# Kernel tuning notes

Measured on AMD Instinct MI355X. Metric: run time of the kernel, lower is better.

The kernel has to match this reference:

```python
import jax, jax.numpy as jnp
import numpy as np

N_ELEC = 64
IN_C = 64
HID = [64, 128]
OUT_C = 128
BATCH = 2048
BN_EPS = 1e-5


def build_graph():
    """Replicates EEGGraphNet._build_graph_structure with random 3D electrode positions."""
    rng = np.random.RandomState(0)
    pos = rng.rand(N_ELEC, 3).astype(np.float64)
    d = np.sqrt(((pos[:, None, :] - pos[None, :, :]) ** 2).sum(-1))
    thr = np.percentile(d[d > 0], 30)
    src, dst = [], []
    for i in range(N_ELEC):
        for j in range(i + 1, N_ELEC):
            if d[i, j] < thr:
                src += [i, j]
                dst += [j, i]
    return np.asarray(src, np.int32), np.asarray(dst, np.int32)


def setup_inputs() -> dict:
    key = jax.random.key(0)
    ks = jax.random.split(key, 8)
    src, dst = build_graph()
    dims = [IN_C] + HID + [OUT_C]  # [64, 64, 128, 128]
    inp = {"x": jax.random.normal(ks[0], (BATCH, N_ELEC, IN_C), jnp.float32)}
    for li in range(3):
        fi, fo = dims[li], dims[li + 1]
        inp[f"W{li+1}"] = jax.random.normal(ks[li + 1], (fi, fo), jnp.float32) * (1.0 / np.sqrt(fi))
        inp[f"b{li+1}"] = jnp.zeros((fo,), jnp.float32)
    for li in range(2):  # BN after first two convs
        inp[f"g{li+1}"] = jnp.ones((dims[li + 1],), jnp.float32)
        inp[f"be{li+1}"] = jnp.zeros((dims[li + 1],), jnp.float32)
    inp["src"] = jnp.asarray(src)
    inp["dst"] = jnp.asarray(dst)
    return inp


def gcn_conv(x, W, b, src, dst, edge_norm, self_norm):
    # x: (B, N, Fin) -> (B, N, Fout). GCN with self-loops, symmetric norm.
    h = jnp.einsum("bnf,fo->bno", x, W)
    msg = h[:, src, :] * edge_norm[None, :, None]          # (B, E, Fout) gather
    agg = jnp.zeros_like(h).at[:, dst, :].add(msg)         # scatter-add over dst
    return agg + h * self_norm[None, :, None] + b


def batchnorm(x, g, be):
    # torch BatchNorm1d over flattened (B*N, C) nodes, training-mode batch stats
    m = jnp.mean(x, axis=(0, 1))
    v = jnp.mean((x - m) ** 2, axis=(0, 1))
    return g * (x - m) * jax.lax.rsqrt(v + BN_EPS) + be


def reference(x, W1, b1, W2, b2, W3, b3, g1, be1, g2, be2, src, dst):
    # degree (with self-loop) is identical across graphs in the batch
    deg = jnp.zeros((N_ELEC,), x.dtype).at[dst].add(1.0) + 1.0
    inv_sqrt = jax.lax.rsqrt(deg)
    edge_norm = inv_sqrt[src] * inv_sqrt[dst]
    self_norm = 1.0 / deg

    h = gcn_conv(x, W1, b1, src, dst, edge_norm, self_norm)
    h = jax.nn.relu(batchnorm(h, g1, be1))
    h = gcn_conv(h, W2, b2, src, dst, edge_norm, self_norm)
    h = jax.nn.relu(batchnorm(h, g2, be2))
    h = gcn_conv(h, W3, b3, src, dst, edge_norm, self_norm)
    return jnp.mean(h, axis=1)  # global mean pool over electrodes -> (B, OUT_C)
```

## Files before the change

kernel.cpp:

```cpp
#include <hip/hip_runtime.h>
#include <hip/hip_bf16.h>

typedef unsigned short ushortT;
typedef unsigned int uintT;
typedef __attribute__((ext_vector_type(8))) short short8;
typedef __attribute__((ext_vector_type(4))) float f32x4;

#define BATCH   2048
#define NELEC   64
#define BN_EPS  1e-5f

#define OFF_AMEAN  4096
#define OFF_SS1    4160
#define OFF_SS2    4288
#define OFF_PS1    4544
#define OFF_PQ1    8640
#define OFF_PS2    12736
#define OFF_PQ2    20928
#define UOFF_A     0
#define UOFF_W1T   9216
#define UOFF_W2T   18432
#define UOFF_H1    36864
#define UOFF_H2    (36864 + 8388608)

#define MFMA(a, b, c) __builtin_amdgcn_mfma_f32_16x16x32_bf16(a, b, c, 0, 0, 0)

__device__ inline float bf2f(ushortT u) { return __uint_as_float(((uintT)u) << 16); }
__device__ inline ushortT f2bf(float f) {
  uintT u = __float_as_uint(f);
  u = (u + 0x7FFFu + ((u >> 16) & 1u)) >> 16;
  return (ushortT)u;
}
__device__ inline void split2(float f, ushortT& hi, ushortT& lo) {
  hi = f2bf(f);
  lo = f2bf(f - bf2f(hi));
}
__device__ inline void splitT8(const float* f, short8& hi, short8& lo) {
  #pragma unroll
  for (int e = 0; e < 8; ++e) {
    uintT u = __float_as_uint(f[e]);
    float fh = __uint_as_float(u & 0xFFFF0000u);
    hi[e] = (short)(u >> 16);
    lo[e] = (short)f2bf(f[e] - fh);
  }
}
__device__ inline uint2 pack4(f32x4 v) {
  uint2 pk;
  pk.x = (uintT)f2bf(v[0]) | ((uintT)f2bf(v[1]) << 16);
  pk.y = (uintT)f2bf(v[2]) | ((uintT)f2bf(v[3]) << 16);
  return pk;
}

__global__ __launch_bounds__(256) void prep_kernel(const int* __restrict__ src,
    const int* __restrict__ dst, int E,
    const float* __restrict__ W1, const float* __restrict__ W2,
    float* __restrict__ ws) {
  __shared__ float degS[NELEC];
  __shared__ float As[NELEC * NELEC];
  int t = threadIdx.x;
  if (t < NELEC) degS[t] = 1.0f;
  for (int i = t; i < NELEC * NELEC; i += 256) As[i] = 0.0f;
  __syncthreads();
  for (int e = t; e < E; e += 256) atomicAdd(&degS[dst[e]], 1.0f);
  __syncthreads();
  for (int e = t; e < E; e += 256) {
    float en = rsqrtf(degS[src[e]]) * rsqrtf(degS[dst[e]]);
    atomicAdd(&As[dst[e] * NELEC + src[e]], en);
  }
  __syncthreads();
  if (t < NELEC) As[t * NELEC + t] += 1.0f / degS[t];
  __syncthreads();
  ushortT* U = (ushortT*)(ws + 29120);
  ushortT* a72 = U + UOFF_A;
  for (int i = t; i < 4096; i += 256) {
    int row = i >> 6, k = i & 63;
    ushortT hi, lo; split2(As[i], hi, lo);
    a72[row * 72 + k] = hi; a72[4608 + row * 72 + k] = lo;
  }
  if (t < NELEC) {
    float s = 0.0f;
    for (int n = 0; n < NELEC; ++n) s += As[n * NELEC + t];
    ws[OFF_AMEAN + t] = s * (1.0f / NELEC);
  }
  ushortT* w1t = U + UOFF_W1T;
  for (int i = t; i < 4096; i += 256) {
    int o = i >> 6, k = i & 63;
    ushortT hi, lo; split2(W1[k * 64 + o], hi, lo);
    w1t[o * 72 + k] = hi; w1t[4608 + o * 72 + k] = lo;
  }
  ushortT* w2t = U + UOFF_W2T;
  for (int i = t; i < 8192; i += 256) {
    int o = i >> 6, k = i & 63;
    ushortT hi, lo; split2(W2[k * 128 + o], hi, lo);
    w2t[o * 72 + k] = hi; w2t[9216 + o * 72 + k] = lo;
  }
}

__global__ __launch_bounds__(512, 2) void layer1_fused(const float* __restrict__ x,
    const float* __restrict__ b1, float* __restrict__ ws) {
  __shared__ ushortT Wl[9216];
  __shared__ ushortT Tt[36864];
  const int t = threadIdx.x;
  ushortT* U = (ushortT*)(ws + 29120);
  for (int i = t; i < 1152; i += 512)
    ((uint4*)Wl)[i] = ((const uint4*)(U + UOFF_W1T))[i];
  const int w = t >> 6, lane = t & 63, c = lane & 15, g = lane >> 4;
  const int b = blockIdx.x * 8 + w;
  short8 Xh[4][2], Xl[4][2];
  #pragma unroll
  for (int nq = 0; nq < 4; ++nq) {
    #pragma unroll
    for (int ks = 0; ks < 2; ++ks) {
      const float* p = x + (size_t)b * 4096 + (nq * 16 + c) * 64 + ks * 32 + g * 8;
      float4 fa = *(const float4*)p, fb = *(const float4*)(p + 4);
      float f[8] = {fa.x, fa.y, fa.z, fa.w, fb.x, fb.y, fb.z, fb.w};
      splitT8(f, Xh[nq][ks], Xl[nq][ks]);
    }
  }
  __syncthreads();
  f32x4 acc[4][4];
  #pragma unroll
  for (int i = 0; i < 4; ++i)
    #pragma unroll
    for (int j = 0; j < 4; ++j) acc[i][j] = (f32x4){0.f, 0.f, 0.f, 0.f};
  #pragma unroll
  for (int ot = 0; ot < 4; ++ot) {
    #pragma unroll
    for (int ks = 0; ks < 2; ++ks) {
      short8 bh = *(const short8*)&Wl[(ot * 16 + c) * 72 + ks * 32 + g * 8];
      short8 bl = *(const short8*)&Wl[4608 + (ot * 16 + c) * 72 + ks * 32 + g * 8];
      #pragma unroll
      for (int nq = 0; nq < 4; ++nq) {
        acc[nq][ot] = MFMA(Xh[nq][ks], bh, acc[nq][ot]);
        acc[nq][ot] = MFMA(Xh[nq][ks], bl, acc[nq][ot]);
        acc[nq][ot] = MFMA(Xl[nq][ks], bh, acc[nq][ot]);
      }
    }
  }
  ushortT* tt = &Tt[w * 4608];
  #pragma unroll
  for (int ot = 0; ot < 4; ++ot)
    #pragma unroll
    for (int nq = 0; nq < 4; ++nq)
      *(uint2*)&tt[(ot * 16 + c) * 72 + nq * 16 + 4 * g] = pack4(acc[nq][ot]);
  short8 ABh[4][2], ABl[4][2];
  #pragma unroll
  for (int sp = 0; sp < 4; ++sp)
    #pragma unroll
    for (int ks = 0; ks < 2; ++ks) {
      ABh[sp][ks] = *(const short8*)(U + (sp * 16 + c) * 72 + ks * 32 + g * 8);
      ABl[sp][ks] = *(const short8*)(U + 4608 + (sp * 16 + c) * 72 + ks * 32 + g * 8);
    }
  f32x4 h[4][4];
  #pragma unroll
  for (int i = 0; i < 4; ++i)
    #pragma unroll
    for (int j = 0; j < 4; ++j) h[i][j] = (f32x4){0.f, 0.f, 0.f, 0.f};
  #pragma unroll
  for (int ks = 0; ks < 2; ++ks) {
    short8 af[4];
    #pragma unroll
    for (int rt = 0; rt < 4; ++rt)
      af[rt] = *(const short8*)&tt[(rt * 16 + c) * 72 + ks * 32 + g * 8];
    #pragma unroll
    for (int sp = 0; sp < 4; ++sp)
      #pragma unroll
      for (int rt = 0; rt < 4; ++rt) {
        h[rt][sp] = MFMA(af[rt], ABh[sp][ks], h[rt][sp]);
        h[rt][sp] = MFMA(af[rt], ABl[sp][ks], h[rt][sp]);
      }
  }
  float Sa[4][4], Qa[4][4];
  #pragma unroll
  for (int i = 0; i < 4; ++i)
    #pragma unroll
    for (int j = 0; j < 4; ++j) { Sa[i][j] = 0.f; Qa[i][j] = 0.f; }
  #pragma unroll
  for (int rt = 0; rt < 4; ++rt) {
    float4 bv = *(const float4*)(b1 + rt * 16 + 4 * g);
    #pragma unroll
    for (int sp = 0; sp < 4; ++sp) {
      f32x4 v;
      v[0] = h[rt][sp][0] + bv.x; v[1] = h[rt][sp][1] + bv.y;
      v[2] = h[rt][sp][2] + bv.z; v[3] = h[rt][sp][3] + bv.w;
      Sa[rt][0] += v[0]; Qa[rt][0] += v[0] * v[0];
      Sa[rt][1] += v[1]; Qa[rt][1] += v[1] * v[1];
      Sa[rt][2] += v[2]; Qa[rt][2] += v[2] * v[2];
      Sa[rt][3] += v[3]; Qa[rt][3] += v[3] * v[3];
      *(uint2*)&tt[(sp * 16 + c) * 72 + rt * 16 + 4 * g] = pack4(v);
    }
  }
  const int slot = blockIdx.x & 63;
  #pragma unroll
  for (int rt = 0; rt < 4; ++rt)
    #pragma unroll
    for (int r = 0; r < 4; ++r) {
      float S = Sa[rt][r], Q = Qa[rt][r];
      S += __shfl_xor(S, 1); S += __shfl_xor(S, 2); S += __shfl_xor(S, 4); S += __shfl_xor(S, 8);
      Q += __shfl_xor(Q, 1); Q += __shfl_xor(Q, 2); Q += __shfl_xor(Q, 4); Q += __shfl_xor(Q, 8);
      if (c == 0) {
        atomicAdd(&ws[OFF_PS1 + slot * 64 + rt * 16 + 4 * g + r], S);
        atomicAdd(&ws[OFF_PQ1 + slot * 64 + rt * 16 + 4 * g + r], Q);
      }
    }
  __syncthreads();
  {
    const int ib = t >> 6, n2 = t & 63;
    const uint4* srcp = (const uint4*)&Tt[ib * 4608 + n2 * 72];
    uint4* dstp = (uint4*)(U + UOFF_H1 + (size_t)(blockIdx.x * 8 + ib) * 4096 + n2 * 64);
    #pragma unroll
    for (int j = 0; j < 8; ++j) dstp[j] = srcp[j];
  }
}

__global__ void reduce1_kernel(const float* __restrict__ g1, const float* __restrict__ be1,
                               float* __restrict__ ws) {
  int t = threadIdx.x;
  if (t < 64) {
    float S = 0.0f, Q = 0.0f;
    for (int s = 0; s < 64; ++s) { S += ws[OFF_PS1 + s * 64 + t]; Q += ws[OFF_PQ1 + s * 64 + t]; }
    const float inv = 1.0f / (float)(BATCH * NELEC);
    float m = S * inv;
    float v = fmaxf(Q * inv - m * m, 0.0f);
    float sc = g1[t] * rsqrtf(v + BN_EPS);
    ws[OFF_SS1 + t] = sc;
    ws[OFF_SS1 + 64 + t] = fmaf(-m, sc, be1[t]);
  }
}

__global__ void reduce2_kernel(const float* __restrict__ g2, const float* __restrict__ be2,
                               float* __restrict__ ws) {
  int t = threadIdx.x;
  if (t < 128) {
    float S = 0.0f, Q = 0.0f;
    for (int s = 0; s < 64; ++s) { S += ws[OFF_PS2 + s * 128 + t]; Q += ws[OFF_PQ2 + s * 128 + t]; }
    const float inv = 1.0f / (float)(BATCH * NELEC);
    float m = S * inv;
    float v = fmaxf(Q * inv - m * m, 0.0f);
    float sc = g2[t] * rsqrtf(v + BN_EPS);
    ws[OFF_SS2 + t] = sc;
    ws[OFF_SS2 + 128 + t] = fmaf(-m, sc, be2[t]);
  }
}

__global__ __launch_bounds__(512, 2) void layer2_fused(const float* __restrict__ b2,
    float* __restrict__ ws) {
  __shared__ ushortT Wl[18432];
  __shared__ ushortT Tt[36864];
  const int t = threadIdx.x;
  ushortT* U = (ushortT*)(ws + 29120);
  for (int i = t; i < 2304; i += 512)
    ((uint4*)Wl)[i] = ((const uint4*)(U + UOFF_W2T))[i];
  const int w = t >> 6, lane = t & 63, c = lane & 15, g = lane >> 4;
  const int b0 = blockIdx.x * 4;
  const ushortT* h1g = U + UOFF_H1;
  float s8[2][8], t8[2][8];
  #pragma unroll
  for (int ks = 0; ks < 2; ++ks) {
    const float* sp_ = ws + OFF_SS1 + ks * 32 + g * 8;
    const float* tp_ = ws + OFF_SS1 + 64 + ks * 32 + g * 8;
    float4 sa = *(const float4*)sp_, sb = *(const float4*)(sp_ + 4);
    float4 ta = *(const float4*)tp_, tb = *(const float4*)(tp_ + 4);
    s8[ks][0]=sa.x; s8[ks][1]=sa.y; s8[ks][2]=sa.z; s8[ks][3]=sa.w;
    s8[ks][4]=sb.x; s8[ks][5]=sb.y; s8[ks][6]=sb.z; s8[ks][7]=sb.w;
    t8[ks][0]=ta.x; t8[ks][1]=ta.y; t8[ks][2]=ta.z; t8[ks][3]=ta.w;
    t8[ks][4]=tb.x; t8[ks][5]=tb.y; t8[ks][6]=tb.z; t8[ks][7]=tb.w;
  }
  short8 Yh[2][2], Yl[2][2];
  #pragma unroll
  for (int si = 0; si < 2; ++si) {
    const int sub = w * 2 + si, ib = sub >> 2, nq = sub & 3;
    #pragma unroll
    for (int ks = 0; ks < 2; ++ks) {
      short8 hv = *(const short8*)(h1g + (size_t)(b0 + ib) * 4096 + (nq * 16 + c) * 64 + ks * 32 + g * 8);
      float f[8];
      #pragma unroll
      for (int e = 0; e < 8; ++e)
        f[e] = fmaxf(fmaf(bf2f((ushortT)hv[e]), s8[ks][e], t8[ks][e]), 0.0f);
      splitT8(f, Yh[si][ks], Yl[si][ks]);
    }
  }
  __syncthreads();
  f32x4 acc[2][8];
  #pragma unroll
  for (int i = 0; i < 2; ++i)
    #pragma unroll
    for (int j = 0; j < 8; ++j) acc[i][j] = (f32x4){0.f, 0.f, 0.f, 0.f};
  #pragma unroll
  for (int ot = 0; ot < 8; ++ot) {
    #pragma unroll
    for (int ks = 0; ks < 2; ++ks) {
      short8 bh = *(const short8*)&Wl[(ot * 16 + c) * 72 + ks * 32 + g * 8];
      short8 bl = *(const short8*)&Wl[9216 + (ot * 16 + c) * 72 + ks * 32 + g * 8];
      #pragma unroll
      for (int si = 0; si < 2; ++si) {
        acc[si][ot] = MFMA(Yh[si][ks], bh, acc[si][ot]);
        acc[si][ot] = MFMA(Yh[si][ks], bl, acc[si][ot]);
        acc[si][ot] = MFMA(Yl[si][ks], bh, acc[si][ot]);
      }
    }
  }
  #pragma unroll
  for (int si = 0; si < 2; ++si) {
    const int sub = w * 2 + si, ib = sub >> 2, nq = sub & 3;
    #pragma unroll
    for (int ot = 0; ot < 8; ++ot)
      *(uint2*)&Tt[ib * 9216 + (ot * 16 + c) * 72 + nq * 16 + 4 * g] = pack4(acc[si][ot]);
  }
  short8 ABh[4][2], ABl[4][2];
  #pragma unroll
  for (int sp = 0; sp < 4; ++sp)
    #pragma unroll
    for (int ks = 0; ks < 2; ++ks) {
      ABh[sp][ks] = *(const short8*)(U + (sp * 16 + c) * 72 + ks * 32 + g * 8);
      ABl[sp][ks] = *(const short8*)(U + 4608 + (sp * 16 + c) * 72 + ks * 32 + g * 8);
    }
  __syncthreads();
  const int ib = w >> 1, oh = w & 1;
  const ushortT* tt = &Tt[ib * 9216];
  f32x4 h[4][4];
  #pragma unroll
  for (int i = 0; i < 4; ++i)
    #pragma unroll
    for (int j = 0; j < 4; ++j) h[i][j] = (f32x4){0.f, 0.f, 0.f, 0.f};
  #pragma unroll
  for (int ks = 0; ks < 2; ++ks) {
    short8 af[4];
    #pragma unroll
    for (int rt = 0; rt < 4; ++rt)
      af[rt] = *(const short8*)&tt[(oh * 64 + rt * 16 + c) * 72 + ks * 32 + g * 8];
    #pragma unroll
    for (int sp = 0; sp < 4; ++sp)
      #pragma unroll
      for (int rt = 0; rt < 4; ++rt) {
        h[rt][sp] = MFMA(af[rt], ABh[sp][ks], h[rt][sp]);
        h[rt][sp] = MFMA(af[rt], ABl[sp][ks], h[rt][sp]);
      }
  }
  float Sa[4][4], Qa[4][4];
  #pragma unroll
  for (int i = 0; i < 4; ++i)
    #pragma unroll
    for (int j = 0; j < 4; ++j) { Sa[i][j] = 0.f; Qa[i][j] = 0.f; }
  #pragma unroll
  for (int rt = 0; rt < 4; ++rt) {
    float4 bv = *(const float4*)(b2 + oh * 64 + rt * 16 + 4 * g);
    #pragma unroll
    for (int sp = 0; sp < 4; ++sp) {
      h[rt][sp][0] += bv.x; h[rt][sp][1] += bv.y;
      h[rt][sp][2] += bv.z; h[rt][sp][3] += bv.w;
      Sa[rt][0] += h[rt][sp][0]; Qa[rt][0] += h[rt][sp][0] * h[rt][sp][0];
      Sa[rt][1] += h[rt][sp][1]; Qa[rt][1] += h[rt][sp][1] * h[rt][sp][1];
      Sa[rt][2] += h[rt][sp][2]; Qa[rt][2] += h[rt][sp][2] * h[rt][sp][2];
      Sa[rt][3] += h[rt][sp][3]; Qa[rt][3] += h[rt][sp][3] * h[rt][sp][3];
    }
  }
  const int slot = blockIdx.x & 63;
  #pragma unroll
  for (int rt = 0; rt < 4; ++rt)
    #pragma unroll
    for (int r = 0; r < 4; ++r) {
      float S = Sa[rt][r], Q = Qa[rt][r];
      S += __shfl_xor(S, 1); S += __shfl_xor(S, 2); S += __shfl_xor(S, 4); S += __shfl_xor(S, 8);
      Q += __shfl_xor(Q, 1); Q += __shfl_xor(Q, 2); Q += __shfl_xor(Q, 4); Q += __shfl_xor(Q, 8);
      if (c == 0) {
        const int ch = oh * 64 + rt * 16 + 4 * g + r;
        atomicAdd(&ws[OFF_PS2 + slot * 128 + ch], S);
        atomicAdd(&ws[OFF_PQ2 + slot * 128 + ch], Q);
      }
    }
  __syncthreads();
  {
    ushortT* hb = &Tt[ib * 9216];
    #pragma unroll
    for (int rt = 0; rt < 4; ++rt)
      #pragma unroll
      for (int sp = 0; sp < 4; ++sp)
        *(uint2*)&hb[(sp * 16 + c) * 136 + oh * 64 + rt * 16 + 4 * g] = pack4(h[rt][sp]);
  }
  __syncthreads();
  {
    const int ib2 = t >> 7, n2 = (t >> 1) & 63, half = t & 1;
    const uint4* srcp = (const uint4*)&Tt[ib2 * 9216 + n2 * 136 + half * 64];
    uint4* dstp = (uint4*)(U + UOFF_H2 + (size_t)(b0 + ib2) * 8192 + n2 * 128 + half * 64);
    #pragma unroll
    for (int j = 0; j < 8; ++j) dstp[j] = srcp[j];
  }
}

__global__ __launch_bounds__(256) void layer3_kernel(const float* __restrict__ W3,
    const float* __restrict__ b3, const float* __restrict__ ws,
    float* __restrict__ out) {
  const int w = threadIdx.x >> 6, lane = threadIdx.x & 63;
  const int item = blockIdx.x * 4 + w;
  const int f0 = lane * 2;
  const float s2a = ws[OFF_SS2 + f0],       s2b = ws[OFF_SS2 + f0 + 1];
  const float t2a = ws[OFF_SS2 + 128 + f0], t2b = ws[OFF_SS2 + 128 + f0 + 1];
  const float* am = ws + OFF_AMEAN;
  const ushortT* h2 = (const ushortT*)(ws + 29120) + UOFF_H2 + (size_t)item * 8192;
  float v0 = 0.0f, v1 = 0.0f;
  #pragma unroll 8
  for (int m = 0; m < 64; ++m) {
    uintT pk = *(const uintT*)(h2 + m * 128 + f0);
    float y0 = fmaxf(fmaf(bf2f((ushortT)(pk & 0xffffu)), s2a, t2a), 0.0f);
    float y1 = fmaxf(fmaf(bf2f((ushortT)(pk >> 16)),     s2b, t2b), 0.0f);
    float a = am[m];
    v0 = fmaf(a, y0, v0);
    v1 = fmaf(a, y1, v1);
  }
  float o0 = b3[f0], o1 = b3[f0 + 1];
  #pragma unroll 8
  for (int k = 0; k < 128; ++k) {
    float vk = __shfl((k & 1) ? v1 : v0, k >> 1, 64);
    o0 = fmaf(vk, W3[k * 128 + f0],     o0);
    o1 = fmaf(vk, W3[k * 128 + f0 + 1], o1);
  }
  float2 ov; ov.x = o0; ov.y = o1;
  *(float2*)(out + (size_t)item * 128 + f0) = ov;
}

extern "C" void kernel_launch(void* const* d_in, const int* in_sizes, int n_in,
                              void* d_out, int out_size, void* d_ws, size_t ws_size,
                              hipStream_t stream) {
  const float* x   = (const float*)d_in[0];
  const float* W1  = (const float*)d_in[1];
  const float* b1  = (const float*)d_in[2];
  const float* W2  = (const float*)d_in[3];
  const float* b2  = (const float*)d_in[4];
  const float* W3  = (const float*)d_in[5];
  const float* b3  = (const float*)d_in[6];
  const float* g1  = (const float*)d_in[7];
  const float* be1 = (const float*)d_in[8];
  const float* g2  = (const float*)d_in[9];
  const float* be2 = (const float*)d_in[10];
  const int*   src = (const int*)d_in[11];
  const int*   dst = (const int*)d_in[12];
  const int E = in_sizes[11];
  float* ws  = (float*)d_ws;
  float* out = (float*)d_out;

  hipMemsetAsync((void*)(ws + OFF_PS1), 0, (size_t)(29120 - OFF_PS1) * 4, stream);
  hipLaunchKernelGGL(prep_kernel,    dim3(1),   dim3(256), 0, stream, src, dst, E, W1, W2, ws);
  hipLaunchKernelGGL(layer1_fused,   dim3(256), dim3(512), 0, stream, x, b1, ws);
  hipLaunchKernelGGL(reduce1_kernel, dim3(1),   dim3(64),  0, stream, g1, be1, ws);
  hipLaunchKernelGGL(layer2_fused,   dim3(512), dim3(512), 0, stream, b2, ws);
  hipLaunchKernelGGL(reduce2_kernel, dim3(1),   dim3(128), 0, stream, g2, be2, ws);
  hipLaunchKernelGGL(layer3_kernel,  dim3(512), dim3(256), 0, stream, W3, b3, ws, out);
}
```

Measured before the change: 186.2 us.

## Split fused GCN layers into separate weight-GEMM, adjacency-GEMM and stats kernels

Each fused layer kernel is split into three kernels. The first does the feature-weight GEMM and writes an intermediate bf16 tensor to global memory. The second does the adjacency GEMM plus bias. The third computes BatchNorm sums in a separate pass with a shared-memory reduction. The goal is smaller blocks with fewer registers and less LDS, giving higher occupancy and fewer atomics, at the cost of extra global round trips and more kernel launches. Layer 3 also stages its pooled vector through shared memory with vectorised W3 loads instead of using shuffles.

Result: slower. 195.6 us (+5.1%).

```diff
diff --git a/kernel.cpp b/kernel.cpp
--- a/kernel.cpp
+++ b/kernel.cpp
@@ -21,7 +21,9 @@
 #define UOFF_W1T   9216
 #define UOFF_W2T   18432
 #define UOFF_H1    36864
-#define UOFF_H2    (36864 + 8388608)
+#define UOFF_H2    8425472
+#define UOFF_T1    25202688
+#define UOFF_T2    25202688
 
 #define MFMA(a, b, c) __builtin_amdgcn_mfma_f32_16x16x32_bf16(a, b, c, 0, 0, 0)
 
@@ -96,31 +98,31 @@
   }
 }
 
-__global__ __launch_bounds__(512, 2) void layer1_fused(const float* __restrict__ x,
-    const float* __restrict__ b1, float* __restrict__ ws) {
+__global__ __launch_bounds__(256, 4) void wgemm1_kernel(const float* __restrict__ x,
+    float* __restrict__ ws) {
   __shared__ ushortT Wl[9216];
-  __shared__ ushortT Tt[36864];
   const int t = threadIdx.x;
   ushortT* U = (ushortT*)(ws + 29120);
-  for (int i = t; i < 1152; i += 512)
+  for (int i = t; i < 1152; i += 256)
     ((uint4*)Wl)[i] = ((const uint4*)(U + UOFF_W1T))[i];
   const int w = t >> 6, lane = t & 63, c = lane & 15, g = lane >> 4;
-  const int b = blockIdx.x * 8 + w;
-  short8 Xh[4][2], Xl[4][2];
-  #pragma unroll
-  for (int nq = 0; nq < 4; ++nq) {
-    #pragma unroll
-    for (int ks = 0; ks < 2; ++ks) {
-      const float* p = x + (size_t)b * 4096 + (nq * 16 + c) * 64 + ks * 32 + g * 8;
+  const int wv = blockIdx.x * 4 + w;
+  const int b = wv >> 1, nh = wv & 1;
+  short8 Xh[2][2], Xl[2][2];
+  #pragma unroll
+  for (int nq = 0; nq < 2; ++nq) {
+    #pragma unroll
+    for (int ks = 0; ks < 2; ++ks) {
+      const float* p = x + (size_t)b * 4096 + ((nh * 2 + nq) * 16 + c) * 64 + ks * 32 + g * 8;
       float4 fa = *(const float4*)p, fb = *(const float4*)(p + 4);
       float f[8] = {fa.x, fa.y, fa.z, fa.w, fb.x, fb.y, fb.z, fb.w};
       splitT8(f, Xh[nq][ks], Xl[nq][ks]);
     }
   }
   __syncthreads();
-  f32x4 acc[4][4];
-  #pragma unroll
-  for (int i = 0; i < 4; ++i)
+  f32x4 acc[2][4];
+  #pragma unroll
+  for (int i = 0; i < 2; ++i)
     #pragma unroll
     for (int j = 0; j < 4; ++j) acc[i][j] = (f32x4){0.f, 0.f, 0.f, 0.f};
   #pragma unroll
@@ -130,86 +132,92 @@
       short8 bh = *(const short8*)&Wl[(ot * 16 + c) * 72 + ks * 32 + g * 8];
       short8 bl = *(const short8*)&Wl[4608 + (ot * 16 + c) * 72 + ks * 32 + g * 8];
       #pragma unroll
-      for (int nq = 0; nq < 4; ++nq) {
+      for (int nq = 0; nq < 2; ++nq) {
         acc[nq][ot] = MFMA(Xh[nq][ks], bh, acc[nq][ot]);
         acc[nq][ot] = MFMA(Xh[nq][ks], bl, acc[nq][ot]);
         acc[nq][ot] = MFMA(Xl[nq][ks], bh, acc[nq][ot]);
       }
     }
   }
-  ushortT* tt = &Tt[w * 4608];
+  ushortT* t1 = U + UOFF_T1 + (size_t)b * 4096;
   #pragma unroll
   for (int ot = 0; ot < 4; ++ot)
     #pragma unroll
-    for (int nq = 0; nq < 4; ++nq)
-      *(uint2*)&tt[(ot * 16 + c) * 72 + nq * 16 + 4 * g] = pack4(acc[nq][ot]);
-  short8 ABh[4][2], ABl[4][2];
-  #pragma unroll
-  for (int sp = 0; sp < 4; ++sp)
-    #pragma unroll
-    for (int ks = 0; ks < 2; ++ks) {
-      ABh[sp][ks] = *(const short8*)(U + (sp * 16 + c) * 72 + ks * 32 + g * 8);
-      ABl[sp][ks] = *(const short8*)(U + 4608 + (sp * 16 + c) * 72 + ks * 32 + g * 8);
-    }
-  f32x4 h[4][4];
-  #pragma unroll
-  for (int i = 0; i < 4; ++i)
-    #pragma unroll
-    for (int j = 0; j < 4; ++j) h[i][j] = (f32x4){0.f, 0.f, 0.f, 0.f};
-  #pragma unroll
-  for (int ks = 0; ks < 2; ++ks) {
-    short8 af[4];
-    #pragma unroll
-    for (int rt = 0; rt < 4; ++rt)
-      af[rt] = *(const short8*)&tt[(rt * 16 + c) * 72 + ks * 32 + g * 8];
-    #pragma unroll
-    for (int sp = 0; sp < 4; ++sp)
+    for (int nq = 0; nq < 2; ++nq)
+      *(uint2*)&t1[(ot * 16 + c) * 64 + (nh * 2 + nq) * 16 + 4 * g] = pack4(acc[nq][ot]);
+}
+
+__global__ __launch_bounds__(256, 4) void agemm1_kernel(const float* __restrict__ b1,
+    float* __restrict__ ws) {
+  const int t = threadIdx.x, w = t >> 6, lane = t & 63, c = lane & 15, g = lane >> 4;
+  const int wv = blockIdx.x * 4 + w;
+  const int b = wv >> 1, oh = wv & 1;
+  ushortT* U = (ushortT*)(ws + 29120);
+  const ushortT* t1 = U + UOFF_T1 + (size_t)b * 4096;
+  short8 tf[2][2];
+  #pragma unroll
+  for (int rt = 0; rt < 2; ++rt)
+    #pragma unroll
+    for (int ks = 0; ks < 2; ++ks)
+      tf[rt][ks] = *(const short8*)(t1 + (oh * 32 + rt * 16 + c) * 64 + ks * 32 + g * 8);
+  float4 bv[2];
+  #pragma unroll
+  for (int rt = 0; rt < 2; ++rt)
+    bv[rt] = *(const float4*)(b1 + oh * 32 + rt * 16 + 4 * g);
+  ushortT* h1 = U + UOFF_H1 + (size_t)b * 4096;
+  #pragma unroll
+  for (int sp = 0; sp < 4; ++sp) {
+    short8 Bh[2], Bl[2];
+    #pragma unroll
+    for (int ks = 0; ks < 2; ++ks) {
+      Bh[ks] = *(const short8*)(U + UOFF_A + (sp * 16 + c) * 72 + ks * 32 + g * 8);
+      Bl[ks] = *(const short8*)(U + UOFF_A + 4608 + (sp * 16 + c) * 72 + ks * 32 + g * 8);
+    }
+    f32x4 acc[2] = {{0.f,0.f,0.f,0.f},{0.f,0.f,0.f,0.f}};
+    #pragma unroll
+    for (int ks = 0; ks < 2; ++ks)
       #pragma unroll
-      for (int rt = 0; rt < 4; ++rt) {
-        h[rt][sp] = MFMA(af[rt], ABh[sp][ks], h[rt][sp]);
-        h[rt][sp] = MFMA(af[rt], ABl[sp][ks], h[rt][sp]);
+      for (int rt = 0; rt < 2; ++rt) {
+        acc[rt] = MFMA(tf[rt][ks], Bh[ks], acc[rt]);
+        acc[rt] = MFMA(tf[rt][ks], Bl[ks], acc[rt]);
       }
-  }
-  float Sa[4][4], Qa[4][4];
-  #pragma unroll
-  for (int i = 0; i < 4; ++i)
-    #pragma unroll
-    for (int j = 0; j < 4; ++j) { Sa[i][j] = 0.f; Qa[i][j] = 0.f; }
-  #pragma unroll
-  for (int rt = 0; rt < 4; ++rt) {
-    float4 bv = *(const float4*)(b1 + rt * 16 + 4 * g);
-    #pragma unroll
-    for (int sp = 0; sp < 4; ++sp) {
-      f32x4 v;
-      v[0] = h[rt][sp][0] + bv.x; v[1] = h[rt][sp][1] + bv.y;
-      v[2] = h[rt][sp][2] + bv.z; v[3] = h[rt][sp][3] + bv.w;
-      Sa[rt][0] += v[0]; Qa[rt][0] += v[0] * v[0];
-      Sa[rt][1] += v[1]; Qa[rt][1] += v[1] * v[1];
-      Sa[rt][2] += v[2]; Qa[rt][2] += v[2] * v[2];
-      Sa[rt][3] += v[3]; Qa[rt][3] += v[3] * v[3];
-      *(uint2*)&tt[(sp * 16 + c) * 72 + rt * 16 + 4 * g] = pack4(v);
-    }
-  }
-  const int slot = blockIdx.x & 63;
-  #pragma unroll
-  for (int rt = 0; rt < 4; ++rt)
-    #pragma unroll
-    for (int r = 0; r < 4; ++r) {
-      float S = Sa[rt][r], Q = Qa[rt][r];
-      S += __shfl_xor(S, 1); S += __shfl_xor(S, 2); S += __shfl_xor(S, 4); S += __shfl_xor(S, 8);
-      Q += __shfl_xor(Q, 1); Q += __shfl_xor(Q, 2); Q += __shfl_xor(Q, 4); Q += __shfl_xor(Q, 8);
-      if (c == 0) {
-        atomicAdd(&ws[OFF_PS1 + slot * 64 + rt * 16 + 4 * g + r], S);
-        atomicAdd(&ws[OFF_PQ1 + slot * 64 + rt * 16 + 4 * g + r], Q);
-      }
-    }
-  __syncthreads();
-  {
-    const int ib = t >> 6, n2 = t & 63;
-    const uint4* srcp = (const uint4*)&Tt[ib * 4608 + n2 * 72];
-    uint4* dstp = (uint4*)(U + UOFF_H1 + (size_t)(blockIdx.x * 8 + ib) * 4096 + n2 * 64);
-    #pragma unroll
-    for (int j = 0; j < 8; ++j) dstp[j] = srcp[j];
+    #pragma unroll
+    for (int rt = 0; rt < 2; ++rt) {
+      acc[rt][0] += bv[rt].x; acc[rt][1] += bv[rt].y;
+      acc[rt][2] += bv[rt].z; acc[rt][3] += bv[rt].w;
+      *(uint2*)&h1[(sp * 16 + c) * 64 + oh * 32 + rt * 16 + 4 * g] = pack4(acc[rt]);
+    }
+  }
+}
+
+__global__ __launch_bounds__(256, 4) void stats1_kernel(float* __restrict__ ws) {
+  __shared__ float P[32 * 128];
+  const int t = threadIdx.x;
+  const int rg = t >> 3, oct = t & 7;
+  const ushortT* h1 = (const ushortT*)(ws + 29120) + UOFF_H1;
+  float S[8] = {}, Q[8] = {};
+  const int r0 = blockIdx.x * 512 + rg * 16;
+  for (int i = 0; i < 16; ++i) {
+    short8 v = *(const short8*)(h1 + (size_t)(r0 + i) * 64 + oct * 8);
+    #pragma unroll
+    for (int e = 0; e < 8; ++e) {
+      float f = bf2f((ushortT)v[e]);
+      S[e] += f; Q[e] += f * f;
+    }
+  }
+  #pragma unroll
+  for (int e = 0; e < 8; ++e) {
+    P[rg * 128 + oct * 8 + e] = S[e];
+    P[rg * 128 + 64 + oct * 8 + e] = Q[e];
+  }
+  __syncthreads();
+  if (t < 128) {
+    float a = 0.f;
+    #pragma unroll
+    for (int r = 0; r < 32; ++r) a += P[r * 128 + t];
+    const int slot = blockIdx.x & 63;
+    if (t < 64) atomicAdd(&ws[OFF_PS1 + slot * 64 + t], a);
+    else        atomicAdd(&ws[OFF_PQ1 + slot * 64 + (t - 64)], a);
   }
 }
 
@@ -243,17 +251,15 @@
   }
 }
 
-__global__ __launch_bounds__(512, 2) void layer2_fused(const float* __restrict__ b2,
-    float* __restrict__ ws) {
+__global__ __launch_bounds__(256, 3) void wgemm2_kernel(float* __restrict__ ws) {
   __shared__ ushortT Wl[18432];
-  __shared__ ushortT Tt[36864];
   const int t = threadIdx.x;
   ushortT* U = (ushortT*)(ws + 29120);
-  for (int i = t; i < 2304; i += 512)
+  for (int i = t; i < 2304; i += 256)
     ((uint4*)Wl)[i] = ((const uint4*)(U + UOFF_W2T))[i];
   const int w = t >> 6, lane = t & 63, c = lane & 15, g = lane >> 4;
-  const int b0 = blockIdx.x * 4;
-  const ushortT* h1g = U + UOFF_H1;
+  const int wv = blockIdx.x * 4 + w;
+  const int b = wv >> 1, nh = wv & 1;
   float s8[2][8], t8[2][8];
   #pragma unroll
   for (int ks = 0; ks < 2; ++ks) {
@@ -266,18 +272,18 @@
     t8[ks][0]=ta.x; t8[ks][1]=ta.y; t8[ks][2]=ta.z; t8[ks][3]=ta.w;
     t8[ks][4]=tb.x; t8[ks][5]=tb.y; t8[ks][6]=tb.z; t8[ks][7]=tb.w;
   }
+  const ushortT* h1 = U + UOFF_H1 + (size_t)b * 4096;
   short8 Yh[2][2], Yl[2][2];
   #pragma unroll
-  for (int si = 0; si < 2; ++si) {
-    const int sub = w * 2 + si, ib = sub >> 2, nq = sub & 3;
-    #pragma unroll
-    for (int ks = 0; ks < 2; ++ks) {
-      short8 hv = *(const short8*)(h1g + (size_t)(b0 + ib) * 4096 + (nq * 16 + c) * 64 + ks * 32 + g * 8);
+  for (int nq = 0; nq < 2; ++nq) {
+    #pragma unroll
+    for (int ks = 0; ks < 2; ++ks) {
+      short8 hv = *(const short8*)(h1 + ((nh * 2 + nq) * 16 + c) * 64 + ks * 32 + g * 8);
       float f[8];
       #pragma unroll
       for (int e = 0; e < 8; ++e)
         f[e] = fmaxf(fmaf(bf2f((ushortT)hv[e]), s8[ks][e], t8[ks][e]), 0.0f);
-      splitT8(f, Yh[si][ks], Yl[si][ks]);
+      splitT8(f, Yh[nq][ks], Yl[nq][ks]);
     }
   }
   __syncthreads();
@@ -293,104 +299,101 @@
       short8 bh = *(const short8*)&Wl[(ot * 16 + c) * 72 + ks * 32 + g * 8];
       short8 bl = *(const short8*)&Wl[9216 + (ot * 16 + c) * 72 + ks * 32 + g * 8];
       #pragma unroll
-      for (int si = 0; si < 2; ++si) {
-        acc[si][ot] = MFMA(Yh[si][ks], bh, acc[si][ot]);
-        acc[si][ot] = MFMA(Yh[si][ks], bl, acc[si][ot]);
-        acc[si][ot] = MFMA(Yl[si][ks], bh, acc[si][ot]);
+      for (int nq = 0; nq < 2; ++nq) {
+        acc[nq][ot] = MFMA(Yh[nq][ks], bh, acc[nq][ot]);
+        acc[nq][ot] = MFMA(Yh[nq][ks], bl, acc[nq][ot]);
+        acc[nq][ot] = MFMA(Yl[nq][ks], bh, acc[nq][ot]);
       }
     }
   }
-  #pragma unroll
-  for (int si = 0; si < 2; ++si) {
-    const int sub = w * 2 + si, ib = sub >> 2, nq = sub & 3;
-    #pragma unroll
-    for (int ot = 0; ot < 8; ++ot)
-      *(uint2*)&Tt[ib * 9216 + (ot * 16 + c) * 72 + nq * 16 + 4 * g] = pack4(acc[si][ot]);
-  }
-  short8 ABh[4][2], ABl[4][2];
-  #pragma unroll
-  for (int sp = 0; sp < 4; ++sp)
-    #pragma unroll
-    for (int ks = 0; ks < 2; ++ks) {
-      ABh[sp][ks] = *(const short8*)(U + (sp * 16 + c) * 72 + ks * 32 + g * 8);
-      ABl[sp][ks] = *(const short8*)(U + 4608 + (sp * 16 + c) * 72 + ks * 32 + g * 8);
-    }
-  __syncthreads();
-  const int ib = w >> 1, oh = w & 1;
-  const ushortT* tt = &Tt[ib * 9216];
-  f32x4 h[4][4];
-  #pragma unroll
-  for (int i = 0; i < 4; ++i)
-    #pragma unroll
-    for (int j = 0; j < 4; ++j) h[i][j] = (f32x4){0.f, 0.f, 0.f, 0.f};
-  #pragma unroll
-  for (int ks = 0; ks < 2; ++ks) {
-    short8 af[4];
-    #pragma unroll
-    for (int rt = 0; rt < 4; ++rt)
-      af[rt] = *(const short8*)&tt[(oh * 64 + rt * 16 + c) * 72 + ks * 32 + g * 8];
-    #pragma unroll
-    for (int sp = 0; sp < 4; ++sp)
+  ushortT* t2 = U + UOFF_T2 + (size_t)b * 8192;
+  #pragma unroll
+  for (int ot = 0; ot < 8; ++ot)
+    #pragma unroll
+    for (int nq = 0; nq < 2; ++nq)
+      *(uint2*)&t2[(ot * 16 + c) * 64 + (nh * 2 + nq) * 16 + 4 * g] = pack4(acc[nq][ot]);
+}
+
+__global__ __launch_bounds__(256, 4) void agemm2_kernel(const float* __restrict__ b2,
+    float* __restrict__ ws) {
+  const int t = threadIdx.x, w = t >> 6, lane = t & 63, c = lane & 15, g = lane >> 4;
+  const int wv = blockIdx.x * 4 + w;
+  const int b = wv >> 1, oh = wv & 1;
+  ushortT* U = (ushortT*)(ws + 29120);
+  const ushortT* t2 = U + UOFF_T2 + (size_t)b * 8192;
+  short8 tf[4][2];
+  #pragma unroll
+  for (int rt = 0; rt < 4; ++rt)
+    #pragma unroll
+    for (int ks = 0; ks < 2; ++ks)
+      tf[rt][ks] = *(const short8*)(t2 + (oh * 64 + rt * 16 + c) * 64 + ks * 32 + g * 8);
+  float4 bv[4];
+  #pragma unroll
+  for (int rt = 0; rt < 4; ++rt)
+    bv[rt] = *(const float4*)(b2 + oh * 64 + rt * 16 + 4 * g);
+  ushortT* h2 = U + UOFF_H2 + (size_t)b * 8192;
+  #pragma unroll
+  for (int sp = 0; sp < 4; ++sp) {
+    short8 Bh[2], Bl[2];
+    #pragma unroll
+    for (int ks = 0; ks < 2; ++ks) {
+      Bh[ks] = *(const short8*)(U + UOFF_A + (sp * 16 + c) * 72 + ks * 32 + g * 8);
+      Bl[ks] = *(const short8*)(U + UOFF_A + 4608 + (sp * 16 + c) * 72 + ks * 32 + g * 8);
+    }
+    f32x4 acc[4];
+    #pragma unroll
+    for (int rt = 0; rt < 4; ++rt) acc[rt] = (f32x4){0.f, 0.f, 0.f, 0.f};
+    #pragma unroll
+    for (int ks = 0; ks < 2; ++ks)
       #pragma unroll
       for (int rt = 0; rt < 4; ++rt) {
-        h[rt][sp] = MFMA(af[rt], ABh[sp][ks], h[rt][sp]);
-        h[rt][sp] = MFMA(af[rt], ABl[sp][ks], h[rt][sp]);
+        acc[rt] = MFMA(tf[rt][ks], Bh[ks], acc[rt]);
+        acc[rt] = MFMA(tf[rt][ks], Bl[ks], acc[rt]);
       }
-  }
-  float Sa[4][4], Qa[4][4];
-  #pragma unroll
-  for (int i = 0; i < 4; ++i)
-    #pragma unroll
-    for (int j = 0; j < 4; ++j) { Sa[i][j] = 0.f; Qa[i][j] = 0.f; }
-  #pragma unroll
-  for (int rt = 0; rt < 4; ++rt) {
-    float4 bv = *(const float4*)(b2 + oh * 64 + rt * 16 + 4 * g);
-    #pragma unroll
-    for (int sp = 0; sp < 4; ++sp) {
-      h[rt][sp][0] += bv.x; h[rt][sp][1] += bv.y;
-      h[rt][sp][2] += bv.z; h[rt][sp][3] += bv.w;
-      Sa[rt][0] += h[rt][sp][0]; Qa[rt][0] += h[rt][sp][0] * h[rt][sp][0];
-      Sa[rt][1] += h[rt][sp][1]; Qa[rt][1] += h[rt][sp][1] * h[rt][sp][1];
-      Sa[rt][2] += h[rt][sp][2]; Qa[rt][2] += h[rt][sp][2] * h[rt][sp][2];
-      Sa[rt][3] += h[rt][sp][3]; Qa[rt][3] += h[rt][sp][3] * h[rt][sp][3];
-    }
-  }
-  const int slot = blockIdx.x & 63;
-  #pragma unroll
-  for (int rt = 0; rt < 4; ++rt)
-    #pragma unroll
-    for (int r = 0; r < 4; ++r) {
-      float S = Sa[rt][r], Q = Qa[rt][r];
-      S += __shfl_xor(S, 1); S += __shfl_xor(S, 2); S += __shfl_xor(S, 4); S += __shfl_xor(S, 8);
-      Q += __shfl_xor(Q, 1); Q += __shfl_xor(Q, 2); Q += __shfl_xor(Q, 4); Q += __shfl_xor(Q, 8);
-      if (c == 0) {
-        const int ch = oh * 64 + rt * 16 + 4 * g + r;
-        atomicAdd(&ws[OFF_PS2 + slot * 128 + ch], S);
-        atomicAdd(&ws[OFF_PQ2 + slot * 128 + ch], Q);
-      }
-    }
+    #pragma unroll
+    for (int rt = 0; rt < 4; ++rt) {
+      acc[rt][0] += bv[rt].x; acc[rt][1] += bv[rt].y;
+      acc[rt][2] += bv[rt].z; acc[rt][3] += bv[rt].w;
+      *(uint2*)&h2[(sp * 16 + c) * 128 + oh * 64 + rt * 16 + 4 * g] = pack4(acc[rt]);
+    }
+  }
+}
+
+__global__ __launch_bounds__(256, 4) void stats2_kernel(float* __restrict__ ws) {
+  __shared__ float P[16 * 256];
+  const int t = threadIdx.x;
+  const int rg = t >> 4, oct = t & 15;
+  const ushortT* h2 = (const ushortT*)(ws + 29120) + UOFF_H2;
+  float S[8] = {}, Q[8] = {};
+  const int r0 = blockIdx.x * 512 + rg * 32;
+  for (int i = 0; i < 32; ++i) {
+    short8 v = *(const short8*)(h2 + (size_t)(r0 + i) * 128 + oct * 8);
+    #pragma unroll
+    for (int e = 0; e < 8; ++e) {
+      float f = bf2f((ushortT)v[e]);
+      S[e] += f; Q[e] += f * f;
+    }
+  }
+  #pragma unroll
+  for (int e = 0; e < 8; ++e) {
+    P[rg * 256 + oct * 8 + e] = S[e];
+    P[rg * 256 + 128 + oct * 8 + e] = Q[e];
+  }
   __syncthreads();
   {
-    ushortT* hb = &Tt[ib * 9216];
-    #pragma unroll
-    for (int rt = 0; rt < 4; ++rt)
-      #pragma unroll
-      for (int sp = 0; sp < 4; ++sp)
-        *(uint2*)&hb[(sp * 16 + c) * 136 + oh * 64 + rt * 16 + 4 * g] = pack4(h[rt][sp]);
-  }
-  __syncthreads();
-  {
-    const int ib2 = t >> 7, n2 = (t >> 1) & 63, half = t & 1;
-    const uint4* srcp = (const uint4*)&Tt[ib2 * 9216 + n2 * 136 + half * 64];
-    uint4* dstp = (uint4*)(U + UOFF_H2 + (size_t)(b0 + ib2) * 8192 + n2 * 128 + half * 64);
-    #pragma unroll
-    for (int j = 0; j < 8; ++j) dstp[j] = srcp[j];
-  }
-}
-
-__global__ __launch_bounds__(256) void layer3_kernel(const float* __restrict__ W3,
+    float a = 0.f;
+    #pragma unroll
+    for (int r = 0; r < 16; ++r) a += P[r * 256 + t];
+    const int slot = blockIdx.x & 63;
+    if (t < 128) atomicAdd(&ws[OFF_PS2 + slot * 128 + t], a);
+    else         atomicAdd(&ws[OFF_PQ2 + slot * 128 + (t - 128)], a);
+  }
+}
+
+__global__ __launch_bounds__(256, 4) void layer3_kernel(const float* __restrict__ W3,
     const float* __restrict__ b3, const float* __restrict__ ws,
     float* __restrict__ out) {
+  __shared__ float vS[4][128];
   const int w = threadIdx.x >> 6, lane = threadIdx.x & 63;
   const int item = blockIdx.x * 4 + w;
   const int f0 = lane * 2;
@@ -408,12 +411,18 @@
     v0 = fmaf(a, y0, v0);
     v1 = fmaf(a, y1, v1);
   }
+  vS[w][f0] = v0; vS[w][f0 + 1] = v1;
   float o0 = b3[f0], o1 = b3[f0 + 1];
   #pragma unroll 8
-  for (int k = 0; k < 128; ++k) {
-    float vk = __shfl((k & 1) ? v1 : v0, k >> 1, 64);
-    o0 = fmaf(vk, W3[k * 128 + f0],     o0);
-    o1 = fmaf(vk, W3[k * 128 + f0 + 1], o1);
+  for (int kq = 0; kq < 32; ++kq) {
+    float4 vk = *(const float4*)&vS[w][kq * 4];
+    #pragma unroll
+    for (int j = 0; j < 4; ++j) {
+      float2 wr = *(const float2*)(W3 + (kq * 4 + j) * 128 + f0);
+      float vj = (j == 0) ? vk.x : (j == 1) ? vk.y : (j == 2) ? vk.z : vk.w;
+      o0 = fmaf(vj, wr.x, o0);
+      o1 = fmaf(vj, wr.y, o1);
+    }
   }
   float2 ov; ov.x = o0; ov.y = o1;
   *(float2*)(out + (size_t)item * 128 + f0) = ov;
@@ -440,10 +449,14 @@
   float* out = (float*)d_out;
 
   hipMemsetAsync((void*)(ws + OFF_PS1), 0, (size_t)(29120 - OFF_PS1) * 4, stream);
-  hipLaunchKernelGGL(prep_kernel,    dim3(1),   dim3(256), 0, stream, src, dst, E, W1, W2, ws);
-  hipLaunchKernelGGL(layer1_fused,   dim3(256), dim3(512), 0, stream, x, b1, ws);
-  hipLaunchKernelGGL(reduce1_kernel, dim3(1),   dim3(64),  0, stream, g1, be1, ws);
-  hipLaunchKernelGGL(layer2_fused,   dim3(512), dim3(512), 0, stream, b2, ws);
-  hipLaunchKernelGGL(reduce2_kernel, dim3(1),   dim3(128), 0, stream, g2, be2, ws);
-  hipLaunchKernelGGL(layer3_kernel,  dim3(512), dim3(256), 0, stream, W3, b3, ws, out);
-}
+  hipLaunchKernelGGL(prep_kernel,    dim3(1),    dim3(256), 0, stream, src, dst, E, W1, W2, ws);
+  hipLaunchKernelGGL(wgemm1_kernel,  dim3(1024), dim3(256), 0, stream, x, ws);
+  hipLaunchKernelGGL(agemm1_kernel,  dim3(1024), dim3(256), 0, stream, b1, ws);
+  hipLaunchKernelGGL(stats1_kernel,  dim3(256),  dim3(256), 0, stream, ws);
+  hipLaunchKernelGGL(reduce1_kernel, dim3(1),    dim3(64),  0, stream, g1, be1, ws);
+  hipLaunchKernelGGL(wgemm2_kernel,  dim3(1024), dim3(256), 0, stream, ws);
+  hipLaunchKernelGGL(agemm2_kernel,  dim3(1024), dim3(256), 0, stream, b2, ws);
+  hipLaunchKernelGGL(stats2_kernel,  dim3(256),  dim3(256), 0, stream, ws);
+  hipLaunchKernelGGL(reduce2_kernel, dim3(1),    dim3(128), 0, stream, g2, be2, ws);
+  hipLaunchKernelGGL(layer3_kernel,  dim3(512),  dim3(256), 0, stream, W3, b3, ws, out);
+}
```
